# Performance work log

Measured on AMD Instinct MI355X. Metric: run time of the kernel, lower is better.

## Reference

```python
import jax, jax.numpy as jnp
import numpy as np

NEG_INF_SCALE = -1e9  # matches mask * -1000000000.0 in the original


def setup_inputs() -> dict:
    key = jax.random.key(0)
    k1, k2, k3, k4 = jax.random.split(key, 4)
    B, H, S, D = 2, 16, 2048, 64
    return {
        "query": jax.random.normal(k1, (B, H, S, D), dtype=jnp.float32),
        "key": jax.random.normal(k2, (B, H, S, D), dtype=jnp.float32),
        "value": jax.random.normal(k3, (B, H, S, D), dtype=jnp.float32),
        "mask": jax.random.randint(k4, (B, 1, 1, S), 0, 2, dtype=jnp.int32),
    }


def reference(query, key, value, mask):
    head_dimension = query.shape[-1]
    scale = 1.0 / jnp.sqrt(jnp.float32(head_dimension))
    # (b h q d),(b h k d) -> (b h q k)
    logits = jnp.einsum("bhqd,bhkd->bhqk", query, key) * scale
    logits = logits + mask.astype(logits.dtype) * NEG_INF_SCALE
    attention_weights = jax.nn.softmax(logits, axis=-1)
    # (b h q k),(b h k d) -> (b h q d)
    output = jnp.einsum("bhqk,bhkd->bhqd", attention_weights, value)
    return output, attention_weights
```

## Files before the change

### kernel.cpp

```cpp
#include <hip/hip_runtime.h>

#define SEQ   2048
#define DIM   64
#define NB    2
#define NH    16
#define NHEAD (NB * NH)
#define BQ    256
#define BK    64
#define NKT   (SEQ / BK)
#define NQT   (SEQ / BQ)
#define QSCALE 0.18033688011112042f

typedef float  f32x4  __attribute__((ext_vector_type(4)));
typedef short  bf16x8 __attribute__((ext_vector_type(8)));
typedef unsigned short u16;
typedef u16    u16x4  __attribute__((ext_vector_type(4)));
typedef u16    u16x8  __attribute__((ext_vector_type(8)));
typedef unsigned int u32x4 __attribute__((ext_vector_type(4)));

__device__ __forceinline__ short f2bf(float x) {
    unsigned u = __float_as_uint(x);
    return (short)((u + 0x7FFFu + ((u >> 16) & 1u)) >> 16);
}

__device__ __forceinline__ unsigned cvtpk(float lo, float hi) {
    unsigned r;
    asm("v_cvt_pk_bf16_f32 %0, %1, %2" : "=v"(r) : "v"(lo), "v"(hi));
    return r;
}

__device__ __forceinline__ void gll16(const void* g, void* l) {
    __builtin_amdgcn_global_load_lds(
        (const __attribute__((address_space(1))) unsigned int*)g,
        (__attribute__((address_space(3))) unsigned int*)l, 16, 0, 0);
}

__global__ __launch_bounds__(256)
void conv_k_kernel(const float* __restrict__ K, u16* __restrict__ Kp)
{
    const int idx  = (int)blockIdx.x * 256 + (int)threadIdx.x;
    const int lane = idx & 63;
    const int s    = (idx >> 6) & 7;
    const int kt   = (idx >> 9) & 31;
    const int h    = idx >> 14;
    const int mrow = lane & 15;
    const int kg4  = (lane >> 4) << 2;
    const int row  = (s >> 1) * 16 + mrow;
    const int cb   = (s & 1) * 32 + kg4;

    const float* src = K + ((size_t)h * SEQ + (size_t)kt * 64 + row) * DIM + cb;
    const float4 a = *reinterpret_cast<const float4*>(src);
    const float4 b = *reinterpret_cast<const float4*>(src + 16);
    u16x8 o;
    o[0] = (u16)f2bf(a.x); o[1] = (u16)f2bf(a.y); o[2] = (u16)f2bf(a.z); o[3] = (u16)f2bf(a.w);
    o[4] = (u16)f2bf(b.x); o[5] = (u16)f2bf(b.y); o[6] = (u16)f2bf(b.z); o[7] = (u16)f2bf(b.w);
    *reinterpret_cast<u16x8*>(Kp + (size_t)idx * 8) = o;
}

__global__ __launch_bounds__(256)
void conv_v_kernel(const float* __restrict__ V, u16* __restrict__ Vp)
{
    const int idx  = (int)blockIdx.x * 256 + (int)threadIdx.x;
    const int lane = idx & 63;
    const int s    = (idx >> 6) & 7;
    const int kt   = (idx >> 9) & 31;
    const int h    = idx >> 14;
    const int mrow = lane & 15;
    const int kg4  = (lane >> 4) << 2;
    const int rd   = (s >> 1) * 16 + mrow;
    const int cb   = (s & 1) * 32 + kg4;

    const float* vb = V + ((size_t)h * SEQ + (size_t)kt * 64) * DIM;
    u16x8 o;
    #pragma unroll
    for (int j = 0; j < 4; ++j) {
        o[j]     = (u16)f2bf(vb[(size_t)(cb + j) * DIM + rd]);
        o[4 + j] = (u16)f2bf(vb[(size_t)(cb + 16 + j) * DIM + rd]);
    }
    *reinterpret_cast<u16x8*>(Vp + (size_t)idx * 8) = o;
}

__global__ __launch_bounds__(1024, 1)
void sdpa_main_kernel(const float* __restrict__ Qp, const u16* __restrict__ Kp,
                      const u16* __restrict__ Vp, const int* __restrict__ Mp,
                      float* __restrict__ Op, float* __restrict__ Pg_)
{
    __shared__ u16   Ks[3][4096];
    __shared__ u16   Vs[3][4096];
    __shared__ float Fb[SEQ];
    __shared__ u16   Pst[16][16][68];

    const int tid  = (int)threadIdx.x;
    const int lane = tid & 63;
    const int w    = tid >> 6;
    const int mrow = lane & 15;
    const int kg4  = (lane >> 4) << 2;

    const int bid  = (int)blockIdx.x;
    const int xcd  = bid & 7;
    const int slot = bid >> 3;
    const int bh   = xcd * 4 + (slot >> 3);
    const int qt   = slot & 7;

    const size_t headoff = (size_t)bh * SEQ * DIM;
    const float* Qg = Qp + headoff + (size_t)qt * BQ * DIM;
    const u16*   Kh = Kp + (size_t)bh * NKT * 4096;
    const u16*   Vh = Vp + (size_t)bh * NKT * 4096;
    const int*   Mg = Mp + (size_t)(bh / NH) * SEQ;
    float*       Og = Op + headoff + (size_t)qt * BQ * DIM;
    float*       Pg = Pg_ + ((size_t)bh * SEQ + (size_t)qt * BQ) * SEQ;

    {
        const int2 m0 = *reinterpret_cast<const int2*>(Mg + tid * 2);
        float2 f0;
        f0.x = m0.x ? -1.0e9f : 0.0f;
        f0.y = m0.y ? -1.0e9f : 0.0f;
        *reinterpret_cast<float2*>(&Fb[tid * 2]) = f0;
    }

    bf16x8 qf0, qf1;
    {
        const float* qrow = Qg + (size_t)(w * 16 + mrow) * DIM;
        const float4 a = *reinterpret_cast<const float4*>(qrow + kg4);
        const float4 b = *reinterpret_cast<const float4*>(qrow + 16 + kg4);
        const float4 c = *reinterpret_cast<const float4*>(qrow + 32 + kg4);
        const float4 d = *reinterpret_cast<const float4*>(qrow + 48 + kg4);
        qf0[0] = f2bf(a.x * QSCALE); qf0[1] = f2bf(a.y * QSCALE);
        qf0[2] = f2bf(a.z * QSCALE); qf0[3] = f2bf(a.w * QSCALE);
        qf0[4] = f2bf(b.x * QSCALE); qf0[5] = f2bf(b.y * QSCALE);
        qf0[6] = f2bf(b.z * QSCALE); qf0[7] = f2bf(b.w * QSCALE);
        qf1[0] = f2bf(c.x * QSCALE); qf1[1] = f2bf(c.y * QSCALE);
        qf1[2] = f2bf(c.z * QSCALE); qf1[3] = f2bf(c.w * QSCALE);
        qf1[4] = f2bf(d.x * QSCALE); qf1[5] = f2bf(d.y * QSCALE);
        qf1[6] = f2bf(d.z * QSCALE); qf1[7] = f2bf(d.w * QSCALE);
    }
    __syncthreads();

    const int so8 = (tid & 511) * 8;
    const int lo8 = lane * 8;

    if (w < 8) {
        gll16(Kh + so8, &Ks[0][so8]);
        gll16(Kh + 4096 + so8, &Ks[1][so8]);
    }

    float lsum = 0.f;
    int bcur = 0, bpre = 2;

    for (int kt = 0; kt < NKT; ++kt) {
        asm volatile("s_waitcnt vmcnt(1)" ::: "memory");
        __builtin_amdgcn_s_barrier();
        if (w < 8)
            gll16(Kh + (size_t)((kt + 2) & (NKT - 1)) * 4096 + so8, &Ks[bpre][so8]);
        __builtin_amdgcn_sched_barrier(0);

        const u16* kp = &Ks[bcur][lo8];
        const int k0 = kt * BK;
        #pragma unroll
        for (int t = 0; t < 4; ++t) {
            const bf16x8 kf0 = *reinterpret_cast<const bf16x8*>(kp + (2 * t) * 512);
            const bf16x8 kf1 = *reinterpret_cast<const bf16x8*>(kp + (2 * t + 1) * 512);
            f32x4 a = {0.f, 0.f, 0.f, 0.f};
            a = __builtin_amdgcn_mfma_f32_16x16x32_bf16(kf0, qf0, a, 0, 0, 0);
            a = __builtin_amdgcn_mfma_f32_16x16x32_bf16(kf1, qf1, a, 0, 0, 0);
            const float4 b = *reinterpret_cast<const float4*>(&Fb[k0 + t * 16 + kg4]);
            lsum += __builtin_amdgcn_exp2f(a[0] + b.x);
            lsum += __builtin_amdgcn_exp2f(a[1] + b.y);
            lsum += __builtin_amdgcn_exp2f(a[2] + b.z);
            lsum += __builtin_amdgcn_exp2f(a[3] + b.w);
        }

        bcur = (bcur == 2) ? 0 : bcur + 1;
        bpre = (bpre == 2) ? 0 : bpre + 1;
    }

    asm volatile("s_waitcnt vmcnt(0)" ::: "memory");

    lsum += __shfl_xor(lsum, 16);
    lsum += __shfl_xor(lsum, 32);
    const float rinv = 1.0f / lsum;

    __builtin_amdgcn_s_barrier();

    f32x4 oacc[4];
    #pragma unroll
    for (int n = 0; n < 4; ++n) {
        oacc[n][0] = 0.f; oacc[n][1] = 0.f; oacc[n][2] = 0.f; oacc[n][3] = 0.f;
    }

    if (w < 8) {
        gll16(Kh + so8, &Ks[0][so8]);
        gll16(Kh + 4096 + so8, &Ks[1][so8]);
    } else {
        gll16(Vh + so8, &Vs[0][so8]);
        gll16(Vh + 4096 + so8, &Vs[1][so8]);
    }
    asm volatile("s_waitcnt vmcnt(1)" ::: "memory");
    __builtin_amdgcn_s_barrier();
    bcur = 0; bpre = 2;

    float* PgW = Pg + (size_t)(w * 16) * SEQ;

    for (int kt = 0; kt < NKT; ++kt) {
        if (kt == 1) { asm volatile("s_waitcnt vmcnt(5)" ::: "memory"); }
        else         { asm volatile("s_waitcnt vmcnt(9)" ::: "memory"); }
        __builtin_amdgcn_s_barrier();
        {
            const size_t nt = (size_t)((kt + 2) & (NKT - 1)) * 4096;
            if (w < 8) gll16(Kh + nt + so8, &Ks[bpre][so8]);
            else       gll16(Vh + nt + so8, &Vs[bpre][so8]);
        }
        __builtin_amdgcn_sched_barrier(0);

        const u16* kp = &Ks[bcur][lo8];
        const u16* vp = &Vs[bcur][lo8];
        const int k0 = kt * BK;
        bf16x8 pf0, pf1;

        #pragma unroll
        for (int half = 0; half < 2; ++half) {
            f32x4 p[2];
            #pragma unroll
            for (int i = 0; i < 2; ++i) {
                const int t = half * 2 + i;
                const bf16x8 kf0 = *reinterpret_cast<const bf16x8*>(kp + (2 * t) * 512);
                const bf16x8 kf1 = *reinterpret_cast<const bf16x8*>(kp + (2 * t + 1) * 512);
                f32x4 a = {0.f, 0.f, 0.f, 0.f};
                a = __builtin_amdgcn_mfma_f32_16x16x32_bf16(kf0, qf0, a, 0, 0, 0);
                a = __builtin_amdgcn_mfma_f32_16x16x32_bf16(kf1, qf1, a, 0, 0, 0);
                const float4 b = *reinterpret_cast<const float4*>(&Fb[k0 + t * 16 + kg4]);
                p[i][0] = __builtin_amdgcn_exp2f(a[0] + b.x) * rinv;
                p[i][1] = __builtin_amdgcn_exp2f(a[1] + b.y) * rinv;
                p[i][2] = __builtin_amdgcn_exp2f(a[2] + b.z) * rinv;
                p[i][3] = __builtin_amdgcn_exp2f(a[3] + b.w) * rinv;
            }
            const u32x4 packed = { cvtpk(p[0][0], p[0][1]), cvtpk(p[0][2], p[0][3]),
                                   cvtpk(p[1][0], p[1][1]), cvtpk(p[1][2], p[1][3]) };
            if (half == 0) pf0 = __builtin_bit_cast(bf16x8, packed);
            else           pf1 = __builtin_bit_cast(bf16x8, packed);
        }

        {
            const u16x4* f0 = reinterpret_cast<const u16x4*>(&pf0);
            const u16x4* f1 = reinterpret_cast<const u16x4*>(&pf1);
            *reinterpret_cast<u16x4*>(&Pst[w][mrow][kg4])      = f0[0];
            *reinterpret_cast<u16x4*>(&Pst[w][mrow][16 + kg4]) = f0[1];
            *reinterpret_cast<u16x4*>(&Pst[w][mrow][32 + kg4]) = f1[0];
            *reinterpret_cast<u16x4*>(&Pst[w][mrow][48 + kg4]) = f1[1];
        }

        #pragma unroll
        for (int n = 0; n < 4; ++n) {
            const bf16x8 vf0 = *reinterpret_cast<const bf16x8*>(vp + (2 * n) * 512);
            const bf16x8 vf1 = *reinterpret_cast<const bf16x8*>(vp + (2 * n + 1) * 512);
            oacc[n] = __builtin_amdgcn_mfma_f32_16x16x32_bf16(pf0, vf0, oacc[n], 0, 0, 0);
            oacc[n] = __builtin_amdgcn_mfma_f32_16x16x32_bf16(pf1, vf1, oacc[n], 0, 0, 0);
        }

        #pragma unroll
        for (int j = 0; j < 4; ++j) {
            const u16x4 r = *reinterpret_cast<const u16x4*>(
                &Pst[w][j * 4 + (lane >> 4)][(lane & 15) * 4]);
            float4 f;
            f.x = __uint_as_float((unsigned)r[0] << 16);
            f.y = __uint_as_float((unsigned)r[1] << 16);
            f.z = __uint_as_float((unsigned)r[2] << 16);
            f.w = __uint_as_float((unsigned)r[3] << 16);
            *reinterpret_cast<float4*>(
                PgW + (size_t)(j * 4 + (lane >> 4)) * SEQ + k0 + 4 * (lane & 15)) = f;
        }

        bcur = (bcur == 2) ? 0 : bcur + 1;
        bpre = (bpre == 2) ? 0 : bpre + 1;
    }

    #pragma unroll
    for (int n = 0; n < 4; ++n) {
        #pragma unroll
        for (int r = 0; r < 4; ++r)
            Og[(size_t)(w * 16 + kg4 + r) * DIM + n * 16 + mrow] = oacc[n][r];
    }
}

extern "C" void kernel_launch(void* const* d_in, const int* in_sizes, int n_in,
                              void* d_out, int out_size, void* d_ws, size_t ws_size,
                              hipStream_t stream) {
    const float* Q = (const float*)d_in[0];
    const float* K = (const float*)d_in[1];
    const float* V = (const float*)d_in[2];
    const int*   M = (const int*)d_in[3];
    float* O = (float*)d_out;
    float* P = O + (size_t)NB * NH * SEQ * DIM;

    u16* Kp = (u16*)d_ws;
    u16* Vp = Kp + (size_t)NHEAD * SEQ * DIM;

    const int conv_blocks = NHEAD * NKT * 8 * 64 / 256;
    conv_k_kernel<<<dim3(conv_blocks), dim3(256), 0, stream>>>(K, Kp);
    conv_v_kernel<<<dim3(conv_blocks), dim3(256), 0, stream>>>(V, Vp);

    sdpa_main_kernel<<<dim3(NHEAD * NQT), dim3(1024, 1, 1), 0, stream>>>(Q, Kp, Vp, M, O, P);
}
```

Measured before the change: 182.3 us.

## Split row-sum pass into separate high-occupancy kernel before attention output pass

Result: slower. 188.0 us (+3.1%).

```diff
diff --git a/kernel.cpp b/kernel.cpp
--- a/kernel.cpp
+++ b/kernel.cpp
@@ -5,10 +5,8 @@
 #define NB    2
 #define NH    16
 #define NHEAD (NB * NH)
-#define BQ    256
 #define BK    64
 #define NKT   (SEQ / BK)
-#define NQT   (SEQ / BQ)
 #define QSCALE 0.18033688011112042f
 
 typedef float  f32x4  __attribute__((ext_vector_type(4)));
@@ -80,15 +78,12 @@
     *reinterpret_cast<u16x8*>(Vp + (size_t)idx * 8) = o;
 }
 
-__global__ __launch_bounds__(1024, 1)
-void sdpa_main_kernel(const float* __restrict__ Qp, const u16* __restrict__ Kp,
-                      const u16* __restrict__ Vp, const int* __restrict__ Mp,
-                      float* __restrict__ Op, float* __restrict__ Pg_)
+__global__ __launch_bounds__(256, 4)
+void sdpa_pass1_kernel(const float* __restrict__ Qp, const u16* __restrict__ Kp,
+                       const int* __restrict__ Mp, float* __restrict__ Op)
 {
     __shared__ u16   Ks[3][4096];
-    __shared__ u16   Vs[3][4096];
     __shared__ float Fb[SEQ];
-    __shared__ u16   Pst[16][16][68];
 
     const int tid  = (int)threadIdx.x;
     const int lane = tid & 63;
@@ -99,23 +94,25 @@
     const int bid  = (int)blockIdx.x;
     const int xcd  = bid & 7;
     const int slot = bid >> 3;
-    const int bh   = xcd * 4 + (slot >> 3);
-    const int qt   = slot & 7;
+    const int bh   = xcd * 4 + (slot >> 5);
+    const int qt   = slot & 31;
 
     const size_t headoff = (size_t)bh * SEQ * DIM;
-    const float* Qg = Qp + headoff + (size_t)qt * BQ * DIM;
+    const float* Qg = Qp + headoff + (size_t)qt * 64 * DIM;
     const u16*   Kh = Kp + (size_t)bh * NKT * 4096;
-    const u16*   Vh = Vp + (size_t)bh * NKT * 4096;
     const int*   Mg = Mp + (size_t)(bh / NH) * SEQ;
-    float*       Og = Op + headoff + (size_t)qt * BQ * DIM;
-    float*       Pg = Pg_ + ((size_t)bh * SEQ + (size_t)qt * BQ) * SEQ;
+    float*       Rv = Op + headoff + (size_t)qt * 64 * DIM;
 
     {
-        const int2 m0 = *reinterpret_cast<const int2*>(Mg + tid * 2);
-        float2 f0;
-        f0.x = m0.x ? -1.0e9f : 0.0f;
-        f0.y = m0.y ? -1.0e9f : 0.0f;
-        *reinterpret_cast<float2*>(&Fb[tid * 2]) = f0;
+        const int4 m0 = *reinterpret_cast<const int4*>(Mg + tid * 8);
+        const int4 m1 = *reinterpret_cast<const int4*>(Mg + tid * 8 + 4);
+        float4 f0, f1;
+        f0.x = m0.x ? -1.0e9f : 0.0f; f0.y = m0.y ? -1.0e9f : 0.0f;
+        f0.z = m0.z ? -1.0e9f : 0.0f; f0.w = m0.w ? -1.0e9f : 0.0f;
+        f1.x = m1.x ? -1.0e9f : 0.0f; f1.y = m1.y ? -1.0e9f : 0.0f;
+        f1.z = m1.z ? -1.0e9f : 0.0f; f1.w = m1.w ? -1.0e9f : 0.0f;
+        *reinterpret_cast<float4*>(&Fb[tid * 8])     = f0;
+        *reinterpret_cast<float4*>(&Fb[tid * 8 + 4]) = f1;
     }
 
     bf16x8 qf0, qf1;
@@ -136,22 +133,25 @@
     }
     __syncthreads();
 
-    const int so8 = (tid & 511) * 8;
+    const int so  = tid * 8;
     const int lo8 = lane * 8;
 
-    if (w < 8) {
-        gll16(Kh + so8, &Ks[0][so8]);
-        gll16(Kh + 4096 + so8, &Ks[1][so8]);
-    }
+    gll16(Kh + so, &Ks[0][so]);
+    gll16(Kh + so + 2048, &Ks[0][so + 2048]);
+    gll16(Kh + 4096 + so, &Ks[1][so]);
+    gll16(Kh + 4096 + so + 2048, &Ks[1][so + 2048]);
 
     float lsum = 0.f;
     int bcur = 0, bpre = 2;
 
     for (int kt = 0; kt < NKT; ++kt) {
-        asm volatile("s_waitcnt vmcnt(1)" ::: "memory");
+        asm volatile("s_waitcnt vmcnt(2)" ::: "memory");
         __builtin_amdgcn_s_barrier();
-        if (w < 8)
-            gll16(Kh + (size_t)((kt + 2) & (NKT - 1)) * 4096 + so8, &Ks[bpre][so8]);
+        {
+            const size_t nt = (size_t)((kt + 2) & (NKT - 1)) * 4096;
+            gll16(Kh + nt + so, &Ks[bpre][so]);
+            gll16(Kh + nt + so + 2048, &Ks[bpre][so + 2048]);
+        }
         __builtin_amdgcn_sched_barrier(0);
 
         const u16* kp = &Ks[bcur][lo8];
@@ -174,13 +174,72 @@
         bpre = (bpre == 2) ? 0 : bpre + 1;
     }
 
-    asm volatile("s_waitcnt vmcnt(0)" ::: "memory");
-
     lsum += __shfl_xor(lsum, 16);
     lsum += __shfl_xor(lsum, 32);
-    const float rinv = 1.0f / lsum;
-
-    __builtin_amdgcn_s_barrier();
+    if (lane < 16)
+        Rv[(size_t)(w * 16 + lane) * DIM] = 1.0f / lsum;
+}
+
+__global__ __launch_bounds__(1024, 1)
+void sdpa_pass2_kernel(const float* __restrict__ Qp, const u16* __restrict__ Kp,
+                       const u16* __restrict__ Vp, const int* __restrict__ Mp,
+                       float* __restrict__ Op, float* __restrict__ Pg_)
+{
+    __shared__ u16   Ks[3][4096];
+    __shared__ u16   Vs[3][4096];
+    __shared__ float Fb[SEQ];
+    __shared__ u16   Pst[16][16][68];
+
+    const int tid  = (int)threadIdx.x;
+    const int lane = tid & 63;
+    const int w    = tid >> 6;
+    const int mrow = lane & 15;
+    const int kg4  = (lane >> 4) << 2;
+
+    const int bid  = (int)blockIdx.x;
+    const int xcd  = bid & 7;
+    const int slot = bid >> 3;
+    const int bh   = xcd * 4 + (slot >> 3);
+    const int qt   = slot & 7;
+
+    const size_t headoff = (size_t)bh * SEQ * DIM;
+    const float* Qg = Qp + headoff + (size_t)qt * 256 * DIM;
+    const u16*   Kh = Kp + (size_t)bh * NKT * 4096;
+    const u16*   Vh = Vp + (size_t)bh * NKT * 4096;
+    const int*   Mg = Mp + (size_t)(bh / NH) * SEQ;
+    float*       Og = Op + headoff + (size_t)qt * 256 * DIM;
+    float*       Pg = Pg_ + ((size_t)bh * SEQ + (size_t)qt * 256) * SEQ;
+
+    const float rinv = Og[(size_t)(w * 16 + mrow) * DIM];
+
+    {
+        const int2 m0 = *reinterpret_cast<const int2*>(Mg + tid * 2);
+        float2 f0;
+        f0.x = m0.x ? -1.0e9f : 0.0f;
+        f0.y = m0.y ? -1.0e9f : 0.0f;
+        *reinterpret_cast<float2*>(&Fb[tid * 2]) = f0;
+    }
+
+    bf16x8 qf0, qf1;
+    {
+        const float* qrow = Qg + (size_t)(w * 16 + mrow) * DIM;
+        const float4 a = *reinterpret_cast<const float4*>(qrow + kg4);
+        const float4 b = *reinterpret_cast<const float4*>(qrow + 16 + kg4);
+        const float4 c = *reinterpret_cast<const float4*>(qrow + 32 + kg4);
+        const float4 d = *reinterpret_cast<const float4*>(qrow + 48 + kg4);
+        qf0[0] = f2bf(a.x * QSCALE); qf0[1] = f2bf(a.y * QSCALE);
+        qf0[2] = f2bf(a.z * QSCALE); qf0[3] = f2bf(a.w * QSCALE);
+        qf0[4] = f2bf(b.x * QSCALE); qf0[5] = f2bf(b.y * QSCALE);
+        qf0[6] = f2bf(b.z * QSCALE); qf0[7] = f2bf(b.w * QSCALE);
+        qf1[0] = f2bf(c.x * QSCALE); qf1[1] = f2bf(c.y * QSCALE);
+        qf1[2] = f2bf(c.z * QSCALE); qf1[3] = f2bf(c.w * QSCALE);
+        qf1[4] = f2bf(d.x * QSCALE); qf1[5] = f2bf(d.y * QSCALE);
+        qf1[6] = f2bf(d.z * QSCALE); qf1[7] = f2bf(d.w * QSCALE);
+    }
+    __syncthreads();
+
+    const int so8 = (tid & 511) * 8;
+    const int lo8 = lane * 8;
 
     f32x4 oacc[4];
     #pragma unroll
@@ -197,7 +256,7 @@
     }
     asm volatile("s_waitcnt vmcnt(1)" ::: "memory");
     __builtin_amdgcn_s_barrier();
-    bcur = 0; bpre = 2;
+    int bcur = 0, bpre = 2;
 
     float* PgW = Pg + (size_t)(w * 16) * SEQ;
 
@@ -299,5 +358,6 @@
     conv_k_kernel<<<dim3(conv_blocks), dim3(256), 0, stream>>>(K, Kp);
     conv_v_kernel<<<dim3(conv_blocks), dim3(256), 0, stream>>>(V, Vp);
 
-    sdpa_main_kernel<<<dim3(NHEAD * NQT), dim3(1024, 1, 1), 0, stream>>>(Q, Kp, Vp, M, O, P);
-}
+    sdpa_pass1_kernel<<<dim3(NHEAD * 32), dim3(256, 1, 1), 0, stream>>>(Q, Kp, M, O);
+    sdpa_pass2_kernel<<<dim3(NHEAD * 8), dim3(1024, 1, 1), 0, stream>>>(Q, Kp, Vp, M, O, P);
+}
```

## Load two K tiles per iteration using both wave groups in the row-sum pass

Applied to the files above, without the earlier changes.

New measurement: 179.9 us. No clear change (-1.3%).

```diff
diff --git a/kernel.cpp b/kernel.cpp
--- a/kernel.cpp
+++ b/kernel.cpp
@@ -141,29 +141,49 @@
 
     if (w < 8) {
         gll16(Kh + so8, &Ks[0][so8]);
-        gll16(Kh + 4096 + so8, &Ks[1][so8]);
+        gll16(Kh + (size_t)2 * 4096 + so8, &Ks[1][so8]);
+    } else {
+        gll16(Kh + (size_t)1 * 4096 + so8, &Vs[0][so8]);
+        gll16(Kh + (size_t)3 * 4096 + so8, &Vs[1][so8]);
     }
 
     float lsum = 0.f;
     int bcur = 0, bpre = 2;
 
-    for (int kt = 0; kt < NKT; ++kt) {
+    for (int j = 0; j < NKT / 2; ++j) {
         asm volatile("s_waitcnt vmcnt(1)" ::: "memory");
         __builtin_amdgcn_s_barrier();
-        if (w < 8)
-            gll16(Kh + (size_t)((kt + 2) & (NKT - 1)) * 4096 + so8, &Ks[bpre][so8]);
+        {
+            const int jn = (j + 2) & (NKT / 2 - 1);
+            if (w < 8) gll16(Kh + (size_t)(2 * jn) * 4096 + so8, &Ks[bpre][so8]);
+            else       gll16(Kh + (size_t)(2 * jn + 1) * 4096 + so8, &Vs[bpre][so8]);
+        }
         __builtin_amdgcn_sched_barrier(0);
 
-        const u16* kp = &Ks[bcur][lo8];
-        const int k0 = kt * BK;
+        const u16* kpe = &Ks[bcur][lo8];
+        const u16* kpo = &Vs[bcur][lo8];
+        const int k0e = (2 * j) * BK;
         #pragma unroll
         for (int t = 0; t < 4; ++t) {
-            const bf16x8 kf0 = *reinterpret_cast<const bf16x8*>(kp + (2 * t) * 512);
-            const bf16x8 kf1 = *reinterpret_cast<const bf16x8*>(kp + (2 * t + 1) * 512);
+            const bf16x8 kf0 = *reinterpret_cast<const bf16x8*>(kpe + (2 * t) * 512);
+            const bf16x8 kf1 = *reinterpret_cast<const bf16x8*>(kpe + (2 * t + 1) * 512);
             f32x4 a = {0.f, 0.f, 0.f, 0.f};
             a = __builtin_amdgcn_mfma_f32_16x16x32_bf16(kf0, qf0, a, 0, 0, 0);
             a = __builtin_amdgcn_mfma_f32_16x16x32_bf16(kf1, qf1, a, 0, 0, 0);
-            const float4 b = *reinterpret_cast<const float4*>(&Fb[k0 + t * 16 + kg4]);
+            const float4 b = *reinterpret_cast<const float4*>(&Fb[k0e + t * 16 + kg4]);
+            lsum += __builtin_amdgcn_exp2f(a[0] + b.x);
+            lsum += __builtin_amdgcn_exp2f(a[1] + b.y);
+            lsum += __builtin_amdgcn_exp2f(a[2] + b.z);
+            lsum += __builtin_amdgcn_exp2f(a[3] + b.w);
+        }
+        #pragma unroll
+        for (int t = 0; t < 4; ++t) {
+            const bf16x8 kf0 = *reinterpret_cast<const bf16x8*>(kpo + (2 * t) * 512);
+            const bf16x8 kf1 = *reinterpret_cast<const bf16x8*>(kpo + (2 * t + 1) * 512);
+            f32x4 a = {0.f, 0.f, 0.f, 0.f};
+            a = __builtin_amdgcn_mfma_f32_16x16x32_bf16(kf0, qf0, a, 0, 0, 0);
+            a = __builtin_amdgcn_mfma_f32_16x16x32_bf16(kf1, qf1, a, 0, 0, 0);
+            const float4 b = *reinterpret_cast<const float4*>(&Fb[k0e + BK + t * 16 + kg4]);
             lsum += __builtin_amdgcn_exp2f(a[0] + b.x);
             lsum += __builtin_amdgcn_exp2f(a[1] + b.y);
             lsum += __builtin_amdgcn_exp2f(a[2] + b.z);
```
